# Kernel optimization log

Hardware: AMD Instinct MI355X
Metric: run time of the kernel (lower is better)

## Reference

```python
import jax, jax.numpy as jnp
import numpy as np

N_NODES = 50000


def _gcn_conv(x, edge_list, edge_attr, W, b):
    # PyG GCNConv with edge_weight: add self loops (weight 1), symmetric norm,
    # h = x @ W, out[dst] += norm * h[src], then + bias.
    n = x.shape[0]
    src, dst = edge_list[0], edge_list[1]
    loop = jnp.arange(n)
    src_f = jnp.concatenate([src, loop])
    dst_f = jnp.concatenate([dst, loop])
    w_f = jnp.concatenate([edge_attr, jnp.ones((n,), dtype=x.dtype)])
    deg = jax.ops.segment_sum(w_f, dst_f, num_segments=n)
    dinv = jnp.where(deg > 0, jax.lax.rsqrt(jnp.where(deg > 0, deg, 1.0)), 0.0)
    norm = dinv[src_f] * w_f * dinv[dst_f]          # [E+N]
    h = x @ W                                        # [N, 64]
    msg = h[src_f] * norm[:, None]                   # [E+N, 64] gather
    out = jax.ops.segment_sum(msg, dst_f, num_segments=n)  # scatter-add
    return out + b


def setup_inputs() -> dict:
    key = jax.random.key(0)
    k1, k2, k3, k4, k5 = jax.random.split(key, 5)
    N, E, F, H = N_NODES, 1_600_000, 128, 64
    x = jax.random.normal(k1, (N, F), dtype=jnp.float32)
    edge_list = jax.random.randint(k2, (2, E), 0, N, dtype=jnp.int64)
    edge_attr = jax.random.uniform(k3, (E,), dtype=jnp.float32)
    conv_w = jax.random.normal(k4, (F, H), dtype=jnp.float32) * (1.0 / np.sqrt(F))
    conv_b = jnp.zeros((H,), dtype=jnp.float32)
    fc_w = jax.random.normal(k5, (N * H,), dtype=jnp.float32) * (1.0 / np.sqrt(N * H))
    fc_b = jnp.zeros((1,), dtype=jnp.float32)
    return {"x": x, "edge_list": edge_list, "edge_attr": edge_attr,
            "conv_w": conv_w, "conv_b": conv_b, "fc_w": fc_w, "fc_b": fc_b}


def reference(x, edge_list, edge_attr, conv_w, conv_b, fc_w, fc_b):
    # training=False: gaussian noise and dropout are no-ops
    h = _gcn_conv(x, edge_list, edge_attr, conv_w, conv_b)
    h = jax.nn.relu(h)
    flat = h.reshape(-1)                       # [N*64]
    logit = jnp.dot(flat, fc_w) + fc_b[0]      # scalar
    return jax.nn.sigmoid(logit)
```

## Files before the change

### kernel.cpp

```cpp
#include <hip/hip_runtime.h>
#include <hip/hip_bf16.h>
#include <math.h>

constexpr int F = 128;
constexpr int H = 64;
constexpr int NB = 32;
constexpr int XS_STRIDE = F + 4;

#define MASK40 ((1ull << 40) - 1)
#define Q24 16777216.0f

__device__ __forceinline__ float blo(unsigned u) { return __uint_as_float(u << 16); }
__device__ __forceinline__ float bhi(unsigned u) { return __uint_as_float(u & 0xffff0000u); }

__global__ __launch_bounds__(256) void k_init(unsigned long long* __restrict__ pk,
                                              int N) {
  int i = blockIdx.x * 256 + threadIdx.x;
  if (i < N) pk[i] = 0ull;
}

__global__ __launch_bounds__(256) void k_count(const int* __restrict__ dst,
                                               const float* __restrict__ w,
                                               unsigned long long* __restrict__ pk,
                                               int* __restrict__ rank, int E) {
  int e = blockIdx.x * 256 + threadIdx.x;
  if (e < E) {
    int d = dst[e];
    unsigned long long enc =
        (1ull << 40) | (unsigned long long)__float2uint_rn(w[e] * Q24);
    unsigned long long old = atomicAdd(&pk[d], enc);
    rank[e] = (int)(old >> 40);
  }
}

__global__ __launch_bounds__(1024) void k_scan1(const unsigned long long* __restrict__ pk,
                                                int* __restrict__ cnt,
                                                float* __restrict__ dinv,
                                                int* __restrict__ cursor,
                                                int* __restrict__ bsum, int N) {
  __shared__ int buf[1024];
  const int t = threadIdx.x;
  const int i = blockIdx.x * 1024 + t;
  int v = 0;
  if (i < N) {
    unsigned long long p = pk[i];
    v = (int)(p >> 40);
    cnt[i] = v;
    dinv[i] = rsqrtf(1.0f + (float)(p & MASK40) * (1.0f / Q24));
  }
  buf[t] = v;
  __syncthreads();
  for (int off = 1; off < 1024; off <<= 1) {
    int add = (t >= off) ? buf[t - off] : 0;
    __syncthreads();
    buf[t] += add;
    __syncthreads();
  }
  if (i < N) cursor[i] = buf[t] - v;
  if (t == 1023) bsum[blockIdx.x] = buf[t];
}

__global__ __launch_bounds__(1024) void k_scan3(int* __restrict__ cursor,
                                                const int* __restrict__ bsum,
                                                int N) {
  __shared__ int off;
  if (threadIdx.x == 0) {
    int s = 0;
    for (int b = 0; b < (int)blockIdx.x; ++b) s += bsum[b];
    off = s;
  }
  __syncthreads();
  int i = blockIdx.x * 1024 + threadIdx.x;
  if (i < N) cursor[i] += off;
}

__global__ __launch_bounds__(256) void k_fill(const int* __restrict__ src,
                                              const int* __restrict__ dst,
                                              const float* __restrict__ w,
                                              const int* __restrict__ rank,
                                              const float* __restrict__ dinv,
                                              const int* __restrict__ cursor,
                                              int2* __restrict__ sorted, int E) {
  int e = blockIdx.x * 256 + threadIdx.x;
  if (e < E) {
    int d = dst[e];
    int s = src[e];
    float sw = dinv[s] * w[e];
    int pos = cursor[d] + rank[e];
    sorted[pos] = make_int2(s, __float_as_int(sw));
  }
}

__global__ __launch_bounds__(256) void k_gemm(const float* __restrict__ x,
                                              const float* __restrict__ W,
                                              unsigned short* __restrict__ hb, int N) {
  __shared__ float Ws[F * H];
  __shared__ float xs[NB * XS_STRIDE];
  const int t = threadIdx.x;
  {
    const float4* W4 = (const float4*)W;
    float4* Ws4 = (float4*)Ws;
#pragma unroll
    for (int i = 0; i < (F * H / 4) / 256; ++i) Ws4[t + i * 256] = W4[t + i * 256];
  }
  const int node0 = blockIdx.x * NB;
  {
    const float4* x4 = (const float4*)(x + (size_t)node0 * F);
    int lim = (N - node0 < NB ? N - node0 : NB) * (F / 4);
    for (int i = t; i < NB * (F / 4); i += 256) {
      int nl = i / (F / 4), kk = i % (F / 4);
      float4 v = (i < lim) ? x4[i] : make_float4(0.f, 0.f, 0.f, 0.f);
      *(float4*)&xs[nl * XS_STRIDE + kk * 4] = v;
    }
  }
  __syncthreads();
  const int f0 = (t & 15) * 4;
  const int nl0 = (t >> 4) * 2;
  float acc[2][4] = {};
  for (int k = 0; k < F; k += 4) {
    float xr[2][4];
    float wr[4][4];
    *(float4*)&xr[0][0] = *(const float4*)&xs[(nl0 + 0) * XS_STRIDE + k];
    *(float4*)&xr[1][0] = *(const float4*)&xs[(nl0 + 1) * XS_STRIDE + k];
#pragma unroll
    for (int i = 0; i < 4; ++i)
      *(float4*)&wr[i][0] = *(const float4*)&Ws[(k + i) * H + f0];
#pragma unroll
    for (int i = 0; i < 4; ++i)
#pragma unroll
      for (int n = 0; n < 2; ++n)
#pragma unroll
        for (int j = 0; j < 4; ++j)
          acc[n][j] += xr[n][i] * wr[i][j];
  }
#pragma unroll
  for (int n = 0; n < 2; ++n) {
    int node = node0 + nl0 + n;
    if (node < N) {
      ushort4 o;
      o.x = __bfloat16_as_ushort(__float2bfloat16(acc[n][0]));
      o.y = __bfloat16_as_ushort(__float2bfloat16(acc[n][1]));
      o.z = __bfloat16_as_ushort(__float2bfloat16(acc[n][2]));
      o.w = __bfloat16_as_ushort(__float2bfloat16(acc[n][3]));
      *(ushort4*)&hb[(size_t)node * H + f0] = o;
    }
  }
}

__global__ __launch_bounds__(256) void k_agg(const int2* __restrict__ sorted,
                                             const int* __restrict__ cursor,
                                             const int* __restrict__ cnt,
                                             const float* __restrict__ dinv,
                                             const unsigned short* __restrict__ hb,
                                             const float* __restrict__ b,
                                             const float* __restrict__ fcw,
                                             float* __restrict__ partials, int N) {
  const int wid = threadIdx.x >> 6;
  const int lane = threadIdx.x & 63;
  const int seg = lane >> 4;
  const int sl = lane & 15;
  const int n = blockIdx.x * 16 + wid * 4 + seg;
  float p = 0.0f;
  if (n < N) {
    float dn = dinv[n];
    uint2 rn = *(const uint2*)(hb + ((size_t)n << 6) + (sl << 2));
    float4 bb = ((const float4*)b)[sl];
    float dn2 = dn * dn;
    float ax = bb.x + dn2 * blo(rn.x);
    float ay = bb.y + dn2 * bhi(rn.x);
    float az = bb.z + dn2 * blo(rn.y);
    float aw = bb.w + dn2 * bhi(rn.y);
    int e = cursor[n];
    int end = e + cnt[n];
    for (; e + 1 < end; e += 2) {
      int2 e0 = sorted[e];
      int2 e1 = sorted[e + 1];
      uint2 r0 = *(const uint2*)(hb + ((size_t)e0.x << 6) + (sl << 2));
      uint2 r1 = *(const uint2*)(hb + ((size_t)e1.x << 6) + (sl << 2));
      float n0 = dn * __int_as_float(e0.y);
      float n1 = dn * __int_as_float(e1.y);
      ax += n0 * blo(r0.x) + n1 * blo(r1.x);
      ay += n0 * bhi(r0.x) + n1 * bhi(r1.x);
      az += n0 * blo(r0.y) + n1 * blo(r1.y);
      aw += n0 * bhi(r0.y) + n1 * bhi(r1.y);
    }
    if (e < end) {
      int2 e0 = sorted[e];
      uint2 r0 = *(const uint2*)(hb + ((size_t)e0.x << 6) + (sl << 2));
      float n0 = dn * __int_as_float(e0.y);
      ax += n0 * blo(r0.x);
      ay += n0 * bhi(r0.x);
      az += n0 * blo(r0.y);
      aw += n0 * bhi(r0.y);
    }
    float4 fw = ((const float4*)fcw)[(size_t)n * 16 + sl];
    p = fmaxf(ax, 0.f) * fw.x + fmaxf(ay, 0.f) * fw.y +
        fmaxf(az, 0.f) * fw.z + fmaxf(aw, 0.f) * fw.w;
  }
  p += __shfl_down(p, 8);
  p += __shfl_down(p, 4);
  p += __shfl_down(p, 2);
  p += __shfl_down(p, 1);
  __shared__ float ls[16];
  if (sl == 0) ls[wid * 4 + seg] = p;
  __syncthreads();
  if (threadIdx.x == 0) {
    float s = 0.f;
#pragma unroll
    for (int i = 0; i < 16; ++i) s += ls[i];
    partials[blockIdx.x] = s;
  }
}

__global__ __launch_bounds__(1024) void k_fred(const float* __restrict__ partials,
                                               int M,
                                               const float* __restrict__ fcb,
                                               float* __restrict__ out) {
  const int t = threadIdx.x;
  float s = 0.0f;
  for (int i = t; i < M; i += 1024) s += partials[i];
#pragma unroll
  for (int off = 32; off > 0; off >>= 1) s += __shfl_down(s, off);
  __shared__ float ls[16];
  if ((t & 63) == 0) ls[t >> 6] = s;
  __syncthreads();
  if (t == 0) {
    float tot = 0.0f;
#pragma unroll
    for (int i = 0; i < 16; ++i) tot += ls[i];
    float logit = tot + fcb[0];
    out[0] = 1.0f / (1.0f + expf(-logit));
  }
}

extern "C" void kernel_launch(void* const* d_in, const int* in_sizes, int n_in,
                              void* d_out, int out_size, void* d_ws, size_t ws_size,
                              hipStream_t stream) {
  const float* x      = (const float*)d_in[0];
  const int*   elist  = (const int*)d_in[1];
  const float* eattr  = (const float*)d_in[2];
  const float* conv_w = (const float*)d_in[3];
  const float* conv_b = (const float*)d_in[4];
  const float* fc_w   = (const float*)d_in[5];
  const float* fc_b   = (const float*)d_in[6];
  float* out = (float*)d_out;

  const int N = in_sizes[0] / F;
  const int E = in_sizes[2];
  const int* src = elist;
  const int* dst = elist + E;

  char* wsb = (char*)d_ws;
  int2*  sorted = (int2*)wsb;
  unsigned long long* pk = (unsigned long long*)(wsb + (size_t)E * 8);
  int*   rank   = (int*)(pk + N);
  unsigned short* hb = (unsigned short*)(rank + E);
  int*   cnt    = (int*)(hb + (size_t)N * H);
  int*   cursor = cnt + N;
  float* dinv   = (float*)(cursor + N);
  float* partials = dinv + N;
  const int nAgg = (N + 15) / 16;
  int* bsum = (int*)(partials + nAgg);
  const int nScan = (N + 1023) / 1024;

  k_init<<<(N + 255) / 256, 256, 0, stream>>>(pk, N);
  k_count<<<(E + 255) / 256, 256, 0, stream>>>(dst, eattr, pk, rank, E);
  k_scan1<<<nScan, 1024, 0, stream>>>(pk, cnt, dinv, cursor, bsum, N);
  k_scan3<<<nScan, 1024, 0, stream>>>(cursor, bsum, N);
  k_gemm<<<(N + NB - 1) / NB, 256, 0, stream>>>(x, conv_w, hb, N);
  k_fill<<<(E + 255) / 256, 256, 0, stream>>>(src, dst, eattr, rank, dinv, cursor,
                                              sorted, E);
  k_agg<<<nAgg, 256, 0, stream>>>(sorted, cursor, cnt, dinv, hb, conv_b, fc_w,
                                  partials, N);
  k_fred<<<1, 1024, 0, stream>>>(partials, nAgg, fc_b, out);
}
```

Before: 268.0 us.

## Merge GEMM with degree counting, fold final reduction into aggregation

Merges the node GEMM and the edge-count atomic pass into one launch using a block-index split, so the two independent stages can overlap on the GPU. The scan's second pass is replaced by a single-thread block-prefix kernel whose offsets are added at use in fill and agg. The aggregation now uses 8 lanes per node with 16-byte loads, and the final sigmoid reduction is done by the last block through an atomic ticket, which removes a kernel launch. The cost is shared-memory allocation on the edge blocks of the merged kernel and nondeterministic float atomic summation order.

```diff
diff --git a/kernel.cpp b/kernel.cpp
--- a/kernel.cpp
+++ b/kernel.cpp
@@ -14,22 +14,81 @@
 __device__ __forceinline__ float bhi(unsigned u) { return __uint_as_float(u & 0xffff0000u); }
 
 __global__ __launch_bounds__(256) void k_init(unsigned long long* __restrict__ pk,
-                                              int N) {
+                                              float* __restrict__ gacc,
+                                              unsigned int* __restrict__ done, int N) {
   int i = blockIdx.x * 256 + threadIdx.x;
   if (i < N) pk[i] = 0ull;
-}
-
-__global__ __launch_bounds__(256) void k_count(const int* __restrict__ dst,
-                                               const float* __restrict__ w,
-                                               unsigned long long* __restrict__ pk,
-                                               int* __restrict__ rank, int E) {
-  int e = blockIdx.x * 256 + threadIdx.x;
-  if (e < E) {
-    int d = dst[e];
-    unsigned long long enc =
-        (1ull << 40) | (unsigned long long)__float2uint_rn(w[e] * Q24);
-    unsigned long long old = atomicAdd(&pk[d], enc);
-    rank[e] = (int)(old >> 40);
+  if (i == 0) { gacc[0] = 0.0f; done[0] = 0u; }
+}
+
+__global__ __launch_bounds__(256) void k_mix(const float* __restrict__ x,
+                                             const float* __restrict__ W,
+                                             unsigned short* __restrict__ hb, int N,
+                                             const int* __restrict__ dst,
+                                             const float* __restrict__ w,
+                                             unsigned long long* __restrict__ pk,
+                                             int* __restrict__ rank, int E, int G) {
+  __shared__ float Ws[F * H];
+  __shared__ float xs[NB * XS_STRIDE];
+  if ((int)blockIdx.x >= G) {
+    int e = ((int)blockIdx.x - G) * 256 + threadIdx.x;
+    if (e < E) {
+      int d = dst[e];
+      unsigned long long enc =
+          (1ull << 40) | (unsigned long long)__float2uint_rn(w[e] * Q24);
+      unsigned long long old = atomicAdd(&pk[d], enc);
+      rank[e] = (int)(old >> 40);
+    }
+    return;
+  }
+  const int t = threadIdx.x;
+  {
+    const float4* W4 = (const float4*)W;
+    float4* Ws4 = (float4*)Ws;
+#pragma unroll
+    for (int i = 0; i < (F * H / 4) / 256; ++i) Ws4[t + i * 256] = W4[t + i * 256];
+  }
+  const int node0 = blockIdx.x * NB;
+  {
+    const float4* x4 = (const float4*)(x + (size_t)node0 * F);
+    int lim = (N - node0 < NB ? N - node0 : NB) * (F / 4);
+    for (int i = t; i < NB * (F / 4); i += 256) {
+      int nl = i / (F / 4), kk = i % (F / 4);
+      float4 v = (i < lim) ? x4[i] : make_float4(0.f, 0.f, 0.f, 0.f);
+      *(float4*)&xs[nl * XS_STRIDE + kk * 4] = v;
+    }
+  }
+  __syncthreads();
+  const int f0 = (t & 15) * 4;
+  const int nl0 = (t >> 4) * 2;
+  float acc[2][4] = {};
+  for (int k = 0; k < F; k += 4) {
+    float xr[2][4];
+    float wr[4][4];
+    *(float4*)&xr[0][0] = *(const float4*)&xs[(nl0 + 0) * XS_STRIDE + k];
+    *(float4*)&xr[1][0] = *(const float4*)&xs[(nl0 + 1) * XS_STRIDE + k];
+#pragma unroll
+    for (int i = 0; i < 4; ++i)
+      *(float4*)&wr[i][0] = *(const float4*)&Ws[(k + i) * H + f0];
+#pragma unroll
+    for (int i = 0; i < 4; ++i)
+#pragma unroll
+      for (int n = 0; n < 2; ++n)
+#pragma unroll
+        for (int j = 0; j < 4; ++j)
+          acc[n][j] += xr[n][i] * wr[i][j];
+  }
+#pragma unroll
+  for (int n = 0; n < 2; ++n) {
+    int node = node0 + nl0 + n;
+    if (node < N) {
+      ushort4 o;
+      o.x = __bfloat16_as_ushort(__float2bfloat16(acc[n][0]));
+      o.y = __bfloat16_as_ushort(__float2bfloat16(acc[n][1]));
+      o.z = __bfloat16_as_ushort(__float2bfloat16(acc[n][2]));
+      o.w = __bfloat16_as_ushort(__float2bfloat16(acc[n][3]));
+      *(ushort4*)&hb[(size_t)node * H + f0] = o;
+    }
   }
 }
 
@@ -60,18 +119,11 @@
   if (t == 1023) bsum[blockIdx.x] = buf[t];
 }
 
-__global__ __launch_bounds__(1024) void k_scan3(int* __restrict__ cursor,
-                                                const int* __restrict__ bsum,
-                                                int N) {
-  __shared__ int off;
+__global__ void k_scan2(const int* __restrict__ bsum, int* __restrict__ bpre, int B) {
   if (threadIdx.x == 0) {
-    int s = 0;
-    for (int b = 0; b < (int)blockIdx.x; ++b) s += bsum[b];
-    off = s;
-  }
-  __syncthreads();
-  int i = blockIdx.x * 1024 + threadIdx.x;
-  if (i < N) cursor[i] += off;
+    int run = 0;
+    for (int b = 0; b < B; ++b) { bpre[b] = run; run += bsum[b]; }
+  }
 }
 
 __global__ __launch_bounds__(256) void k_fill(const int* __restrict__ src,
@@ -80,156 +132,100 @@
                                               const int* __restrict__ rank,
                                               const float* __restrict__ dinv,
                                               const int* __restrict__ cursor,
+                                              const int* __restrict__ bpre,
                                               int2* __restrict__ sorted, int E) {
   int e = blockIdx.x * 256 + threadIdx.x;
   if (e < E) {
     int d = dst[e];
     int s = src[e];
     float sw = dinv[s] * w[e];
-    int pos = cursor[d] + rank[e];
+    int pos = cursor[d] + bpre[d >> 10] + rank[e];
     sorted[pos] = make_int2(s, __float_as_int(sw));
-  }
-}
-
-__global__ __launch_bounds__(256) void k_gemm(const float* __restrict__ x,
-                                              const float* __restrict__ W,
-                                              unsigned short* __restrict__ hb, int N) {
-  __shared__ float Ws[F * H];
-  __shared__ float xs[NB * XS_STRIDE];
-  const int t = threadIdx.x;
-  {
-    const float4* W4 = (const float4*)W;
-    float4* Ws4 = (float4*)Ws;
-#pragma unroll
-    for (int i = 0; i < (F * H / 4) / 256; ++i) Ws4[t + i * 256] = W4[t + i * 256];
-  }
-  const int node0 = blockIdx.x * NB;
-  {
-    const float4* x4 = (const float4*)(x + (size_t)node0 * F);
-    int lim = (N - node0 < NB ? N - node0 : NB) * (F / 4);
-    for (int i = t; i < NB * (F / 4); i += 256) {
-      int nl = i / (F / 4), kk = i % (F / 4);
-      float4 v = (i < lim) ? x4[i] : make_float4(0.f, 0.f, 0.f, 0.f);
-      *(float4*)&xs[nl * XS_STRIDE + kk * 4] = v;
-    }
-  }
-  __syncthreads();
-  const int f0 = (t & 15) * 4;
-  const int nl0 = (t >> 4) * 2;
-  float acc[2][4] = {};
-  for (int k = 0; k < F; k += 4) {
-    float xr[2][4];
-    float wr[4][4];
-    *(float4*)&xr[0][0] = *(const float4*)&xs[(nl0 + 0) * XS_STRIDE + k];
-    *(float4*)&xr[1][0] = *(const float4*)&xs[(nl0 + 1) * XS_STRIDE + k];
-#pragma unroll
-    for (int i = 0; i < 4; ++i)
-      *(float4*)&wr[i][0] = *(const float4*)&Ws[(k + i) * H + f0];
-#pragma unroll
-    for (int i = 0; i < 4; ++i)
-#pragma unroll
-      for (int n = 0; n < 2; ++n)
-#pragma unroll
-        for (int j = 0; j < 4; ++j)
-          acc[n][j] += xr[n][i] * wr[i][j];
-  }
-#pragma unroll
-  for (int n = 0; n < 2; ++n) {
-    int node = node0 + nl0 + n;
-    if (node < N) {
-      ushort4 o;
-      o.x = __bfloat16_as_ushort(__float2bfloat16(acc[n][0]));
-      o.y = __bfloat16_as_ushort(__float2bfloat16(acc[n][1]));
-      o.z = __bfloat16_as_ushort(__float2bfloat16(acc[n][2]));
-      o.w = __bfloat16_as_ushort(__float2bfloat16(acc[n][3]));
-      *(ushort4*)&hb[(size_t)node * H + f0] = o;
-    }
   }
 }
 
 __global__ __launch_bounds__(256) void k_agg(const int2* __restrict__ sorted,
                                              const int* __restrict__ cursor,
+                                             const int* __restrict__ bpre,
                                              const int* __restrict__ cnt,
                                              const float* __restrict__ dinv,
                                              const unsigned short* __restrict__ hb,
                                              const float* __restrict__ b,
                                              const float* __restrict__ fcw,
-                                             float* __restrict__ partials, int N) {
+                                             float* __restrict__ gacc,
+                                             unsigned int* __restrict__ done,
+                                             const float* __restrict__ fcb,
+                                             float* __restrict__ out,
+                                             int N, int nBlocks) {
   const int wid = threadIdx.x >> 6;
   const int lane = threadIdx.x & 63;
-  const int seg = lane >> 4;
-  const int sl = lane & 15;
-  const int n = blockIdx.x * 16 + wid * 4 + seg;
+  const int seg = lane >> 3;
+  const int sl = lane & 7;
+  const int n = blockIdx.x * 32 + wid * 8 + seg;
+  const uint4* h4 = (const uint4*)hb;
   float p = 0.0f;
   if (n < N) {
     float dn = dinv[n];
-    uint2 rn = *(const uint2*)(hb + ((size_t)n << 6) + (sl << 2));
-    float4 bb = ((const float4*)b)[sl];
     float dn2 = dn * dn;
-    float ax = bb.x + dn2 * blo(rn.x);
-    float ay = bb.y + dn2 * bhi(rn.x);
-    float az = bb.z + dn2 * blo(rn.y);
-    float aw = bb.w + dn2 * bhi(rn.y);
-    int e = cursor[n];
+    uint4 rn = h4[(size_t)n * 8 + sl];
+    float4 b0 = ((const float4*)b)[sl * 2];
+    float4 b1 = ((const float4*)b)[sl * 2 + 1];
+    float a0 = b0.x + dn2 * blo(rn.x), a1 = b0.y + dn2 * bhi(rn.x);
+    float a2 = b0.z + dn2 * blo(rn.y), a3 = b0.w + dn2 * bhi(rn.y);
+    float a4 = b1.x + dn2 * blo(rn.z), a5 = b1.y + dn2 * bhi(rn.z);
+    float a6 = b1.z + dn2 * blo(rn.w), a7 = b1.w + dn2 * bhi(rn.w);
+    int e = cursor[n] + bpre[n >> 10];
     int end = e + cnt[n];
     for (; e + 1 < end; e += 2) {
       int2 e0 = sorted[e];
       int2 e1 = sorted[e + 1];
-      uint2 r0 = *(const uint2*)(hb + ((size_t)e0.x << 6) + (sl << 2));
-      uint2 r1 = *(const uint2*)(hb + ((size_t)e1.x << 6) + (sl << 2));
+      uint4 r0 = h4[(size_t)e0.x * 8 + sl];
+      uint4 r1 = h4[(size_t)e1.x * 8 + sl];
       float n0 = dn * __int_as_float(e0.y);
       float n1 = dn * __int_as_float(e1.y);
-      ax += n0 * blo(r0.x) + n1 * blo(r1.x);
-      ay += n0 * bhi(r0.x) + n1 * bhi(r1.x);
-      az += n0 * blo(r0.y) + n1 * blo(r1.y);
-      aw += n0 * bhi(r0.y) + n1 * bhi(r1.y);
+      a0 += n0 * blo(r0.x) + n1 * blo(r1.x);
+      a1 += n0 * bhi(r0.x) + n1 * bhi(r1.x);
+      a2 += n0 * blo(r0.y) + n1 * blo(r1.y);
+      a3 += n0 * bhi(r0.y) + n1 * bhi(r1.y);
+      a4 += n0 * blo(r0.z) + n1 * blo(r1.z);
+      a5 += n0 * bhi(r0.z) + n1 * bhi(r1.z);
+      a6 += n0 * blo(r0.w) + n1 * blo(r1.w);
+      a7 += n0 * bhi(r0.w) + n1 * bhi(r1.w);
     }
     if (e < end) {
       int2 e0 = sorted[e];
-      uint2 r0 = *(const uint2*)(hb + ((size_t)e0.x << 6) + (sl << 2));
+      uint4 r0 = h4[(size_t)e0.x * 8 + sl];
       float n0 = dn * __int_as_float(e0.y);
-      ax += n0 * blo(r0.x);
-      ay += n0 * bhi(r0.x);
-      az += n0 * blo(r0.y);
-      aw += n0 * bhi(r0.y);
-    }
-    float4 fw = ((const float4*)fcw)[(size_t)n * 16 + sl];
-    p = fmaxf(ax, 0.f) * fw.x + fmaxf(ay, 0.f) * fw.y +
-        fmaxf(az, 0.f) * fw.z + fmaxf(aw, 0.f) * fw.w;
-  }
-  p += __shfl_down(p, 8);
+      a0 += n0 * blo(r0.x); a1 += n0 * bhi(r0.x);
+      a2 += n0 * blo(r0.y); a3 += n0 * bhi(r0.y);
+      a4 += n0 * blo(r0.z); a5 += n0 * bhi(r0.z);
+      a6 += n0 * blo(r0.w); a7 += n0 * bhi(r0.w);
+    }
+    float4 f0 = ((const float4*)fcw)[(size_t)n * 16 + sl * 2];
+    float4 f1 = ((const float4*)fcw)[(size_t)n * 16 + sl * 2 + 1];
+    p = fmaxf(a0, 0.f) * f0.x + fmaxf(a1, 0.f) * f0.y +
+        fmaxf(a2, 0.f) * f0.z + fmaxf(a3, 0.f) * f0.w +
+        fmaxf(a4, 0.f) * f1.x + fmaxf(a5, 0.f) * f1.y +
+        fmaxf(a6, 0.f) * f1.z + fmaxf(a7, 0.f) * f1.w;
+  }
   p += __shfl_down(p, 4);
   p += __shfl_down(p, 2);
   p += __shfl_down(p, 1);
-  __shared__ float ls[16];
-  if (sl == 0) ls[wid * 4 + seg] = p;
+  __shared__ float ls[32];
+  if (sl == 0) ls[wid * 8 + seg] = p;
   __syncthreads();
   if (threadIdx.x == 0) {
     float s = 0.f;
 #pragma unroll
-    for (int i = 0; i < 16; ++i) s += ls[i];
-    partials[blockIdx.x] = s;
-  }
-}
-
-__global__ __launch_bounds__(1024) void k_fred(const float* __restrict__ partials,
-                                               int M,
-                                               const float* __restrict__ fcb,
-                                               float* __restrict__ out) {
-  const int t = threadIdx.x;
-  float s = 0.0f;
-  for (int i = t; i < M; i += 1024) s += partials[i];
-#pragma unroll
-  for (int off = 32; off > 0; off >>= 1) s += __shfl_down(s, off);
-  __shared__ float ls[16];
-  if ((t & 63) == 0) ls[t >> 6] = s;
-  __syncthreads();
-  if (t == 0) {
-    float tot = 0.0f;
-#pragma unroll
-    for (int i = 0; i < 16; ++i) tot += ls[i];
-    float logit = tot + fcb[0];
-    out[0] = 1.0f / (1.0f + expf(-logit));
+    for (int i = 0; i < 32; ++i) s += ls[i];
+    atomicAdd(gacc, s);
+    __threadfence();
+    unsigned int ticket = atomicAdd(done, 1u);
+    if (ticket == (unsigned int)(nBlocks - 1)) {
+      float tot = atomicAdd(gacc, 0.0f);
+      float logit = tot + fcb[0];
+      out[0] = 1.0f / (1.0f + expf(-logit));
+    }
   }
 }
 
@@ -258,19 +254,22 @@
   int*   cnt    = (int*)(hb + (size_t)N * H);
   int*   cursor = cnt + N;
   float* dinv   = (float*)(cursor + N);
-  float* partials = dinv + N;
-  const int nAgg = (N + 15) / 16;
-  int* bsum = (int*)(partials + nAgg);
   const int nScan = (N + 1023) / 1024;
-
-  k_init<<<(N + 255) / 256, 256, 0, stream>>>(pk, N);
-  k_count<<<(E + 255) / 256, 256, 0, stream>>>(dst, eattr, pk, rank, E);
+  int*   bsum   = (int*)(dinv + N);
+  int*   bpre   = bsum + nScan;
+  float* gacc   = (float*)(bpre + nScan);
+  unsigned int* done = (unsigned int*)(gacc + 1);
+
+  const int G = (N + NB - 1) / NB;
+  const int C = (E + 255) / 256;
+  const int nAgg = (N + 31) / 32;
+
+  k_init<<<(N + 255) / 256, 256, 0, stream>>>(pk, gacc, done, N);
+  k_mix<<<G + C, 256, 0, stream>>>(x, conv_w, hb, N, dst, eattr, pk, rank, E, G);
   k_scan1<<<nScan, 1024, 0, stream>>>(pk, cnt, dinv, cursor, bsum, N);
-  k_scan3<<<nScan, 1024, 0, stream>>>(cursor, bsum, N);
-  k_gemm<<<(N + NB - 1) / NB, 256, 0, stream>>>(x, conv_w, hb, N);
+  k_scan2<<<1, 64, 0, stream>>>(bsum, bpre, nScan);
   k_fill<<<(E + 255) / 256, 256, 0, stream>>>(src, dst, eattr, rank, dinv, cursor,
-                                              sorted, E);
-  k_agg<<<nAgg, 256, 0, stream>>>(sorted, cursor, cnt, dinv, hb, conv_b, fc_w,
-                                  partials, N);
-  k_fred<<<1, 1024, 0, stream>>>(partials, nAgg, fc_b, out);
-}
+                                              bpre, sorted, E);
+  k_agg<<<nAgg, 256, 0, stream>>>(sorted, cursor, bpre, cnt, dinv, hb, conv_b, fc_w,
+                                  gacc, done, fc_b, out, N, nAgg);
+}
```

Measured after the change: 285.7 us. +6.6%, slower.
